# Kernel tuning notes

Measured on AMD Instinct MI355X. Metric: run time of the kernel, lower is better.

## Reference

```python
import jax, jax.numpy as jnp
import numpy as np

DIM = 256; SEQ = 2048; WIN = 64; HEADS = 4; RANK = 32; LAYERS = 3; VOCAB = 32000
EPS = 1e-6

def _unit(v):
    # unit_normalize_values: project onto unit sphere along feature dim
    return v / jnp.maximum(jnp.linalg.norm(v, axis=-1, keepdims=True), EPS)

def _signed_softmax(s):
    # signed_softmax_state: sign(s) * softmax(|s|) over nodes
    return jnp.sign(s) * jax.nn.softmax(jnp.abs(s), axis=-1)

def setup_inputs() -> dict:
    key = jax.random.key(0)
    ks = jax.random.split(key, 10)
    d = DIM
    return {
        "input_ids": jax.random.randint(ks[0], (2, SEQ), 0, VOCAB, dtype=jnp.int32),
        "emb": 0.02 * jax.random.normal(ks[1], (VOCAB, d), jnp.float32),
        "pos_emb": 0.02 * jax.random.normal(ks[2], (SEQ, d), jnp.float32),
        "anchor_val": 0.02 * jax.random.normal(ks[3], (d,), jnp.float32),
        "anchor_state": jnp.zeros((), jnp.float32),
        "Ws": 0.02 * jax.random.normal(ks[4], (d,), jnp.float32),
        "bs": jnp.zeros((), jnp.float32),
        "U": 0.02 * jax.random.normal(ks[5], (LAYERS, d, HEADS, RANK), jnp.float32),
        "V": 0.02 * jax.random.normal(ks[6], (LAYERS, d, HEADS, RANK), jnp.float32),
        "W1": 0.02 * jax.random.normal(ks[7], (LAYERS, d, 2 * d), jnp.float32),
        "b1": jnp.zeros((LAYERS, 2 * d), jnp.float32),
        "W2": 0.02 * jax.random.normal(ks[8], (LAYERS, 2 * d, d), jnp.float32),
        "b2": jnp.zeros((LAYERS, d), jnp.float32),
    }

def _forward(emb, pos_emb, anchor_val, anchor_state, Ws, bs, U, V, W1, b1, W2, b2, input_ids):
    B, S = input_ids.shape
    tok = emb[input_ids] + pos_emb[None, :S]          # [B,S,D]
    state_src = tok                                    # state projected from pre-unit-norm values
    tok = _unit(tok)
    tstate = state_src @ Ws + bs                       # [B,S] scalar state per node
    val = jnp.concatenate([jnp.broadcast_to(_unit(anchor_val), (B, 1, DIM)), tok], axis=1)
    state = jnp.concatenate([jnp.broadcast_to(anchor_state, (B, 1)), tstate], axis=1)
    N = S + 1
    offs = jnp.arange(-WIN, WIN + 1)
    idx = jnp.arange(N)[:, None] + offs[None, :]       # [N,K]
    valid = (idx >= 0) & (idx < N)
    idxc = jnp.clip(idx, 0, N - 1)
    inv_sqrt_r = np.float32(1.0 / np.sqrt(RANK))
    for l in range(LAYERS):
        q = jnp.einsum('bnd,dhr->bnhr', val, U[l])
        k = jnp.einsum('bnd,dhr->bnhr', val, V[l])
        knb = k[:, idxc]                               # [B,N,K,H,R] window gather
        s = jnp.einsum('bnhr,bnkhr->bnkh', q, knb) * inv_sqrt_r
        s = s.max(axis=-1)                             # max head-aggregate [B,N,K]
        a = jnp.where(valid, jnp.abs(s), -jnp.inf)
        wgt = jnp.where(valid, jnp.sign(s) * jax.nn.softmax(a, axis=-1), 0.0)  # signed-abs-softmax edges
        dval = jnp.einsum('bnk,bnkd->bnd', wgt, val[:, idxc])
        dstate = jnp.sum(wgt * state[:, idxc], axis=-1)
        # apply_delta: residual + norm(identity) + unit-norm + touched-mask where
        updated = val + dval
        nv = _unit(updated)
        touched = jnp.max(jnp.abs(jax.lax.stop_gradient(dval)), axis=-1, keepdims=True) > 0
        val = jnp.where(touched, nv, updated)
        state = _signed_softmax(state + dstate)
        # residual feed-forward then re-unit-norm
        h = jax.nn.gelu(jnp.einsum('bnd,dh->bnh', val, W1[l]) + b1[l], approximate=False)
        val = _unit(val + jnp.einsum('bnh,hd->bnd', h, W2[l]) + b2[l])
    return state, val

def reference(input_ids, emb, pos_emb, anchor_val, anchor_state, Ws, bs, U, V, W1, b1, W2, b2):
    return _forward(emb, pos_emb, anchor_val, anchor_state, Ws, bs, U, V, W1, b1, W2, b2, input_ids)
```

## Files before the change

### kernel.cpp

```cpp
#include <hip/hip_runtime.h>
#include <hip/hip_bf16.h>
#include <math.h>

#define BB 2
#define SS 2048
#define NN 2049
#define MM (BB*NN)
#define DD 256
#define HR 128
#define NHEAD 4
#define WINW 64
#define DFF 512
#define EPSF 1e-6f
#define TB8 257

typedef __attribute__((ext_vector_type(8))) short bf16x8;
typedef __attribute__((ext_vector_type(4))) float f32x4;

__device__ __forceinline__ float wave_sum(float v) {
    v += __shfl_down(v, 32, 64); v += __shfl_down(v, 16, 64);
    v += __shfl_down(v, 8, 64);  v += __shfl_down(v, 4, 64);
    v += __shfl_down(v, 2, 64);  v += __shfl_down(v, 1, 64);
    return v;
}
__device__ __forceinline__ float wave_max(float v) {
    v = fmaxf(v, __shfl_down(v, 32, 64)); v = fmaxf(v, __shfl_down(v, 16, 64));
    v = fmaxf(v, __shfl_down(v, 8, 64));  v = fmaxf(v, __shfl_down(v, 4, 64));
    v = fmaxf(v, __shfl_down(v, 2, 64));  v = fmaxf(v, __shfl_down(v, 1, 64));
    return v;
}
__device__ __forceinline__ float block_sum(float v, float* red) {
    v = wave_sum(v);
    __syncthreads();
    if ((threadIdx.x & 63) == 0) red[threadIdx.x >> 6] = v;
    __syncthreads();
    return red[0] + red[1] + red[2] + red[3];
}
__device__ __forceinline__ float sgnf(float x) {
    return (x > 0.f) ? 1.f : ((x < 0.f) ? -1.f : 0.f);
}
__device__ __forceinline__ ushort f2b(float x) {
    __hip_bfloat16 h = __float2bfloat16(x);
    return *(ushort*)&h;
}
__device__ __forceinline__ float b2f(ushort u) {
    unsigned int v = ((unsigned int)u) << 16;
    return *(float*)&v;
}
__device__ __forceinline__ void split3(float x, ushort& h, ushort& m, ushort& l) {
    h = f2b(x);
    float r1 = x - b2f(h);
    m = f2b(r1);
    l = f2b(r1 - b2f(m));
}
__device__ __forceinline__ void pack_map(int e, int N, int& k, int& n) {
    int j = e & 7;
    int l = (e >> 3) & 63;
    int c = e >> 9;
    int ntiles = N >> 4;
    int kt = c / ntiles, nt = c - kt * ntiles;
    k = kt * 32 + ((l >> 4) << 3) + j;
    n = nt * 16 + (l & 15);
}
__device__ __forceinline__ void dma16(const ushort* g, ushort* lds) {
    __builtin_amdgcn_global_load_lds(
        (const __attribute__((address_space(1))) unsigned int*)g,
        (__attribute__((address_space(3))) unsigned int*)lds,
        16, 0, 0);
}

__global__ void pre_kernel(const int* __restrict__ ids,
                           const float* __restrict__ emb,
                           const float* __restrict__ pos,
                           const float* __restrict__ anchor_val,
                           const float* __restrict__ anchor_state,
                           const float* __restrict__ Ws,
                           const float* __restrict__ bs,
                           float* __restrict__ val,
                           float* __restrict__ state,
                           const float* __restrict__ W1, const float* __restrict__ W2,
                           const float* __restrict__ U,  const float* __restrict__ V,
                           ushort* __restrict__ W1ph, ushort* __restrict__ W1pl,
                           ushort* __restrict__ W2ph, ushort* __restrict__ W2pl,
                           ushort* __restrict__ U0, ushort* __restrict__ U1,
                           ushort* __restrict__ U2,
                           ushort* __restrict__ V0, ushort* __restrict__ V1,
                           ushort* __restrict__ V2) {
    __shared__ float red[4];
    int bid = blockIdx.x;
    int t = threadIdx.x;
    if (bid < MM) {
        int b = bid / NN, n = bid % NN;
        float e;
        if (n == 0) {
            e = anchor_val[t];
        } else {
            int id = ids[b * SS + (n - 1)];
            e = emb[(size_t)id * DD + t] + pos[(size_t)(n - 1) * DD + t];
        }
        float ss = block_sum(e * e, red);
        float ts = block_sum(e * Ws[t], red);
        float rn = 1.f / fmaxf(sqrtf(ss), EPSF);
        float o = e * rn;
        val[(size_t)bid * DD + t] = o;
        if (t == 0) state[bid] = (n == 0) ? anchor_state[0] : (ts + bs[0]);
        return;
    }
    int idx = (bid - MM) * 256 + t;
    int l = idx / 327680;
    int r = idx - l * 327680;
    if (l >= 3) return;
    int k, n;
    if (r < 131072) {
        int e = r;
        pack_map(e, 512, k, n);
        float s = W1[(size_t)l * 131072 + (size_t)k * 512 + n];
        ushort h = f2b(s);
        W1ph[(size_t)l * 131072 + e] = h;
        W1pl[(size_t)l * 131072 + e] = f2b(s - b2f(h));
    } else if (r < 262144) {
        int e = r - 131072;
        pack_map(e, 256, k, n);
        float s = W2[(size_t)l * 131072 + (size_t)k * 256 + n];
        ushort h = f2b(s);
        W2ph[(size_t)l * 131072 + e] = h;
        W2pl[(size_t)l * 131072 + e] = f2b(s - b2f(h));
    } else if (r < 294912) {
        int e = r - 262144;
        pack_map(e, 128, k, n);
        ushort h, m, lo;
        split3(U[(size_t)l * 32768 + (size_t)k * 128 + n], h, m, lo);
        U0[(size_t)l * 32768 + e] = h;
        U1[(size_t)l * 32768 + e] = m;
        U2[(size_t)l * 32768 + e] = lo;
    } else {
        int e = r - 294912;
        pack_map(e, 128, k, n);
        ushort h, m, lo;
        split3(V[(size_t)l * 32768 + (size_t)k * 128 + n], h, m, lo);
        V0[(size_t)l * 32768 + e] = h;
        V1[(size_t)l * 32768 + e] = m;
        V2[(size_t)l * 32768 + e] = lo;
    }
}

__global__ __launch_bounds__(256, 2)
void proj_kernel(const float* __restrict__ Xin,
                 const ushort* __restrict__ U0, const ushort* __restrict__ U1,
                 const ushort* __restrict__ U2,
                 const ushort* __restrict__ V0, const ushort* __restrict__ V1,
                 const ushort* __restrict__ V2,
                 ushort* __restrict__ q0, ushort* __restrict__ q1,
                 ushort* __restrict__ q2,
                 ushort* __restrict__ k0, ushort* __restrict__ k1,
                 ushort* __restrict__ k2,
                 float* __restrict__ valG, int donorm) {
    __shared__ __align__(16) ushort stage[2][24 * 512];
    __shared__ __align__(16) ushort pln[3][16 * 256];
    int t = threadIdx.x;
    int w = t >> 6, l = t & 63;
    int lm = l & 15, quad = l >> 4;
    int m0 = blockIdx.x * 16;
    bool isQ = (blockIdx.y == 0);
    const ushort* P[3];
    P[0] = isQ ? U0 : V0;
    P[1] = isQ ? U1 : V1;
    P[2] = isQ ? U2 : V2;

    #pragma unroll
    for (int i = 0; i < 6; i++) {
        int c = w * 6 + i;
        int p = c >> 3, ntl = c & 7;
        dma16(P[p] + ((size_t)ntl * 64 + l) * 8,
              &stage[0][c * 512 + l * 8]);
    }
    asm volatile("" ::: "memory");

    #pragma unroll
    for (int rr = 0; rr < 4; rr++) {
        int row = w * 4 + rr;
        int tok = m0 + row; if (tok > MM - 1) tok = MM - 1;
        f32x4 x = *(const f32x4*)(Xin + (size_t)tok * DD + l * 4);
        if (donorm) {
            float s = x[0]*x[0] + x[1]*x[1] + x[2]*x[2] + x[3]*x[3];
            #pragma unroll
            for (int off = 1; off < 64; off <<= 1) s += __shfl_xor(s, off, 64);
            float rn = 1.f / fmaxf(sqrtf(s), EPSF);
            x[0] *= rn; x[1] *= rn; x[2] *= rn; x[3] *= rn;
            if (isQ) *(f32x4*)(valG + (size_t)tok * DD + l * 4) = x;
        }
        ushort4 h4, m4, l4;
        ushort hh, mm, ll;
        split3(x[0], hh, mm, ll); h4.x = hh; m4.x = mm; l4.x = ll;
        split3(x[1], hh, mm, ll); h4.y = hh; m4.y = mm; l4.y = ll;
        split3(x[2], hh, mm, ll); h4.z = hh; m4.z = mm; l4.z = ll;
        split3(x[3], hh, mm, ll); h4.w = hh; m4.w = mm; l4.w = ll;
        unsigned byte = ((unsigned)(row * 512 + l * 8)) ^ ((unsigned)((row & 7) << 4));
        *(ushort4*)((char*)&pln[0][0] + byte) = h4;
        *(ushort4*)((char*)&pln[1][0] + byte) = m4;
        *(ushort4*)((char*)&pln[2][0] + byte) = l4;
    }
    __syncthreads();

    f32x4 acc[2];
    acc[0] = (f32x4)(0.f); acc[1] = (f32x4)(0.f);
    #pragma unroll
    for (int kt = 0; kt < 8; kt++) {
        int cur = kt & 1;
        if (kt < 7) {
            #pragma unroll
            for (int i = 0; i < 6; i++) {
                int c = w * 6 + i;
                int p = c >> 3, ntl = c & 7;
                dma16(P[p] + ((size_t)((kt + 1) * 8 + ntl) * 64 + l) * 8,
                      &stage[cur ^ 1][c * 512 + l * 8]);
            }
            asm volatile("s_waitcnt vmcnt(6)" ::: "memory");
        } else {
            asm volatile("s_waitcnt vmcnt(0)" ::: "memory");
        }
        __builtin_amdgcn_s_barrier();
        unsigned abyte = ((unsigned)(lm * 512 + kt * 64 + quad * 16)) ^
                         ((unsigned)((lm & 7) << 4));
        bf16x8 a0 = *(const bf16x8*)((char*)&pln[0][0] + abyte);
        bf16x8 a1 = *(const bf16x8*)((char*)&pln[1][0] + abyte);
        bf16x8 a2 = *(const bf16x8*)((char*)&pln[2][0] + abyte);
        #pragma unroll
        for (int jj = 0; jj < 2; jj++) {
            int ntl = w * 2 + jj;
            bf16x8 b0 = *(const bf16x8*)&stage[cur][(0 * 8 + ntl) * 512 + l * 8];
            bf16x8 b1 = *(const bf16x8*)&stage[cur][(1 * 8 + ntl) * 512 + l * 8];
            bf16x8 b2 = *(const bf16x8*)&stage[cur][(2 * 8 + ntl) * 512 + l * 8];
            acc[jj] = __builtin_amdgcn_mfma_f32_16x16x32_bf16(a0, b0, acc[jj], 0, 0, 0);
            acc[jj] = __builtin_amdgcn_mfma_f32_16x16x32_bf16(a0, b1, acc[jj], 0, 0, 0);
            acc[jj] = __builtin_amdgcn_mfma_f32_16x16x32_bf16(a1, b0, acc[jj], 0, 0, 0);
            acc[jj] = __builtin_amdgcn_mfma_f32_16x16x32_bf16(a1, b1, acc[jj], 0, 0, 0);
            acc[jj] = __builtin_amdgcn_mfma_f32_16x16x32_bf16(a0, b2, acc[jj], 0, 0, 0);
            acc[jj] = __builtin_amdgcn_mfma_f32_16x16x32_bf16(a2, b0, acc[jj], 0, 0, 0);
        }
        __builtin_amdgcn_s_barrier();
    }
    ushort* o0 = isQ ? q0 : k0;
    ushort* o1 = isQ ? q1 : k1;
    ushort* o2 = isQ ? q2 : k2;
    #pragma unroll
    for (int jj = 0; jj < 2; jj++) {
        int n = (w * 2 + jj) * 16 + lm;
        #pragma unroll
        for (int r = 0; r < 4; r++) {
            int tok = m0 + quad * 4 + r;
            if (tok < MM) {
                ushort h, m, lo;
                split3(acc[jj][r], h, m, lo);
                size_t oi = (size_t)tok * HR + n;
                o0[oi] = h; o1[oi] = m; o2[oi] = lo;
            }
        }
    }
}

__global__ __launch_bounds__(256, 2)
void attn_kernel(const float* __restrict__ val_in,
                 const float* __restrict__ state_in,
                 const ushort* __restrict__ q0, const ushort* __restrict__ q1,
                 const ushort* __restrict__ q2,
                 const ushort* __restrict__ k0, const ushort* __restrict__ k1,
                 const ushort* __restrict__ k2,
                 float* __restrict__ val_out,
                 ushort* __restrict__ vbH, ushort* __restrict__ vbM,
                 float* __restrict__ dstate_out) {
    __shared__ float sc4[NHEAD][8][148];
    __shared__ float wgt2[144][12];
    __shared__ float redS[8][4];
    __shared__ float redM[8][4];

    int b = blockIdx.x / TB8;
    int n0 = (blockIdx.x % TB8) * 8;
    int t = threadIdx.x;
    int w = t >> 6, l = t & 63;
    int lm = l & 15, quad = l >> 4;

    {
        int qrow = n0 + (lm & 7);
        if (qrow > NN - 1) qrow = NN - 1;
        size_t qa = ((size_t)(b * NN + qrow)) * HR + w * 32 + quad * 8;
        bf16x8 a0 = *(const bf16x8*)(q0 + qa);
        bf16x8 a1 = *(const bf16x8*)(q1 + qa);
        bf16x8 a2 = *(const bf16x8*)(q2 + qa);
        bf16x8 kf0[9], kf1[9], kf2[9];
        #pragma unroll
        for (int jt = 0; jt < 9; jt++) {
            int j = n0 - 64 + jt * 16 + lm;
            j = (j < 0) ? 0 : ((j > NN - 1) ? NN - 1 : j);
            size_t ka = ((size_t)(b * NN + j)) * HR + w * 32 + quad * 8;
            kf0[jt] = *(const bf16x8*)(k0 + ka);
            kf1[jt] = *(const bf16x8*)(k1 + ka);
            kf2[jt] = *(const bf16x8*)(k2 + ka);
        }
        #pragma unroll
        for (int jt = 0; jt < 9; jt++) {
            f32x4 acc = (f32x4)(0.f);
            acc = __builtin_amdgcn_mfma_f32_16x16x32_bf16(a0, kf0[jt], acc, 0, 0, 0);
            acc = __builtin_amdgcn_mfma_f32_16x16x32_bf16(a0, kf1[jt], acc, 0, 0, 0);
            acc = __builtin_amdgcn_mfma_f32_16x16x32_bf16(a1, kf0[jt], acc, 0, 0, 0);
            acc = __builtin_amdgcn_mfma_f32_16x16x32_bf16(a1, kf1[jt], acc, 0, 0, 0);
            acc = __builtin_amdgcn_mfma_f32_16x16x32_bf16(a0, kf2[jt], acc, 0, 0, 0);
            acc = __builtin_amdgcn_mfma_f32_16x16x32_bf16(a2, kf0[jt], acc, 0, 0, 0);
            if (quad < 2) {
                #pragma unroll
                for (int r = 0; r < 4; r++)
                    sc4[w][quad * 4 + r][jt * 16 + lm] = acc[r];
            }
        }
    }
    __syncthreads();

    {
        int m = t >> 5, p = t & 31;
        int n = n0 + m;
        bool tokv = (n < NN);
        float sv[5]; bool vv[5];
        float mx = -INFINITY;
        #pragma unroll
        for (int i = 0; i < 5; i++) {
            int tap = p + 32 * i;
            bool inb = (tap < 144);
            int tapc = inb ? tap : 0;
            int j = n0 - 64 + tapc;
            float s0 = sc4[0][m][tapc], s1 = sc4[1][m][tapc];
            float s2 = sc4[2][m][tapc], s3 = sc4[3][m][tapc];
            float s = fmaxf(fmaxf(s0, s1), fmaxf(s2, s3)) * 0.17677669529663687f;
            bool v = inb && tokv && (tap >= m) && (tap <= m + 128) && (j >= 0) && (j < NN);
            sv[i] = s; vv[i] = v;
            if (v) mx = fmaxf(mx, fabsf(s));
        }
        for (int off = 16; off > 0; off >>= 1) mx = fmaxf(mx, __shfl_xor(mx, off, 64));
        float ee[5];
        float sum = 0.f;
        #pragma unroll
        for (int i = 0; i < 5; i++) {
            ee[i] = vv[i] ? expf(fabsf(sv[i]) - mx) : 0.f;
            sum += ee[i];
        }
        for (int off = 16; off > 0; off >>= 1) sum += __shfl_xor(sum, off, 64);
        float inv = (sum > 0.f) ? 1.f / sum : 0.f;
        float ds = 0.f;
        #pragma unroll
        for (int i = 0; i < 5; i++) {
            int tap = p + 32 * i;
            if (tap < 144) {
                float wg = vv[i] ? sgnf(sv[i]) * ee[i] * inv : 0.f;
                wgt2[tap][m] = wg;
                if (vv[i]) ds += wg * state_in[b * NN + (n0 - 64 + tap)];
            }
        }
        for (int off = 16; off > 0; off >>= 1) ds += __shfl_xor(ds, off, 64);
        if (p == 0 && tokv) dstate_out[b * NN + n] = ds;
    }
    __syncthreads();

    {
        int d = (t >> 2) * 4;
        int tg = t & 3;
        int tok0 = tg * 2, tok1 = tg * 2 + 1;
        int jlo = (n0 >= 64) ? 0 : (64 - n0);
        int jhi = NN - 1 - n0 + 64; if (jhi > 135) jhi = 135;
        const float* vbase = val_in + ((size_t)(b * NN + n0 - 64)) * DD + d;
        f32x4 acc0 = (f32x4)(0.f), acc1 = (f32x4)(0.f);
        int jj = jlo;
        for (; jj + 3 <= jhi; jj += 4) {
            f32x4 v0 = *(const f32x4*)(vbase + (size_t)(jj + 0) * DD);
            f32x4 v1 = *(const f32x4*)(vbase + (size_t)(jj + 1) * DD);
            f32x4 v2 = *(const f32x4*)(vbase + (size_t)(jj + 2) * DD);
            f32x4 v3 = *(const f32x4*)(vbase + (size_t)(jj + 3) * DD);
            float wa0 = wgt2[jj + 0][tok0], wa1 = wgt2[jj + 0][tok1];
            float wb0 = wgt2[jj + 1][tok0], wb1 = wgt2[jj + 1][tok1];
            float wc0 = wgt2[jj + 2][tok0], wc1 = wgt2[jj + 2][tok1];
            float wd0 = wgt2[jj + 3][tok0], wd1 = wgt2[jj + 3][tok1];
            #pragma unroll
            for (int c = 0; c < 4; c++) {
                acc0[c] += v0[c] * wa0 + v1[c] * wb0 + v2[c] * wc0 + v3[c] * wd0;
                acc1[c] += v0[c] * wa1 + v1[c] * wb1 + v2[c] * wc1 + v3[c] * wd1;
            }
        }
        for (; jj <= jhi; jj++) {
            f32x4 v = *(const f32x4*)(vbase + (size_t)jj * DD);
            float w0 = wgt2[jj][tok0], w1 = wgt2[jj][tok1];
            #pragma unroll
            for (int c = 0; c < 4; c++) {
                acc0[c] += v[c] * w0;
                acc1[c] += v[c] * w1;
            }
        }
        f32x4 u[2]; f32x4 ac[2]; ac[0] = acc0; ac[1] = acc1;
        #pragma unroll
        for (int ti = 0; ti < 2; ti++) {
            int tok = tg * 2 + ti;
            int n = n0 + tok;
            f32x4 vold = (f32x4)(0.f);
            if (n < NN) vold = *(const f32x4*)(val_in + ((size_t)(b * NN + n)) * DD + d);
            u[ti] = vold + ac[ti];
            float s = u[ti][0]*u[ti][0] + u[ti][1]*u[ti][1] + u[ti][2]*u[ti][2] + u[ti][3]*u[ti][3];
            float mb = fmaxf(fmaxf(fabsf(ac[ti][0]), fabsf(ac[ti][1])),
                             fmaxf(fabsf(ac[ti][2]), fabsf(ac[ti][3])));
            for (int off = 4; off <= 32; off <<= 1) {
                s += __shfl_xor(s, off, 64);
                mb = fmaxf(mb, __shfl_xor(mb, off, 64));
            }
            if ((l >> 2) == 0) { redS[tok][w] = s; redM[tok][w] = mb; }
        }
        __syncthreads();
        #pragma unroll
        for (int ti = 0; ti < 2; ti++) {
            int tok = tg * 2 + ti;
            int n = n0 + tok;
            if (n < NN) {
                float ss = redS[tok][0] + redS[tok][1] + redS[tok][2] + redS[tok][3];
                float mab = fmaxf(fmaxf(redM[tok][0], redM[tok][1]),
                                  fmaxf(redM[tok][2], redM[tok][3]));
                float rn = 1.f / fmaxf(sqrtf(ss), EPSF);
                f32x4 o = u[ti];
                if (mab > 0.f) { o[0] *= rn; o[1] *= rn; o[2] *= rn; o[3] *= rn; }
                size_t oi = ((size_t)(b * NN + n)) * DD + d;
                *(f32x4*)(val_out + oi) = o;
                ushort4 hv, mv;
                {
                    ushort h0 = f2b(o[0]); hv.x = h0; mv.x = f2b(o[0] - b2f(h0));
                    ushort h1 = f2b(o[1]); hv.y = h1; mv.y = f2b(o[1] - b2f(h1));
                    ushort h2 = f2b(o[2]); hv.z = h2; mv.z = f2b(o[2] - b2f(h2));
                    ushort h3 = f2b(o[3]); hv.w = h3; mv.w = f2b(o[3] - b2f(h3));
                }
                *(ushort4*)(vbH + oi) = hv;
                *(ushort4*)(vbM + oi) = mv;
            }
        }
    }
}

__global__ __launch_bounds__(256, 2)
void ffn1_kernel(const ushort* __restrict__ XbH, const ushort* __restrict__ XbM,
                 const ushort* __restrict__ W1h, const ushort* __restrict__ W1l,
                 const float*  __restrict__ b1,
                 ushort* __restrict__ Hh, ushort* __restrict__ Hl,
                 const float* __restrict__ state_in, const float* __restrict__ dstate,
                 float* __restrict__ state_out) {
    __shared__ __align__(16) ushort stage[2][32 * 512];
    int t = threadIdx.x;

    if (blockIdx.x == 257) {
        float* red = (float*)&stage[0][0];
        int b = blockIdx.y;
        float lmax = -INFINITY;
        for (int n = t; n < NN; n += 256) {
            float x = state_in[b * NN + n] + dstate[b * NN + n];
            lmax = fmaxf(lmax, fabsf(x));
        }
        lmax = wave_max(lmax);
        if ((t & 63) == 0) red[t >> 6] = lmax;
        __syncthreads();
        float m = fmaxf(fmaxf(red[0], red[1]), fmaxf(red[2], red[3]));
        float lsum = 0.f;
        for (int n = t; n < NN; n += 256)
            lsum += expf(fabsf(state_in[b * NN + n] + dstate[b * NN + n]) - m);
        lsum = wave_sum(lsum);
        __syncthreads();
        if ((t & 63) == 0) red[4 + (t >> 6)] = lsum;
        __syncthreads();
        float inv = 1.f / (red[4] + red[5] + red[6] + red[7]);
        for (int n = t; n < NN; n += 256) {
            float x = state_in[b * NN + n] + dstate[b * NN + n];
            state_out[b * NN + n] = sgnf(x) * expf(fabsf(x) - m) * inv;
        }
        return;
    }

    int w = t >> 6, l = t & 63;
    int lm = l & 15, quad = l >> 4;
    int m0 = blockIdx.x * 16;
    int nh = blockIdx.y;
    int row0 = m0 + lm; if (row0 > MM - 1) row0 = MM - 1;
    const ushort* xh = XbH + (size_t)row0 * DD + quad * 8;
    const ushort* xm = XbM + (size_t)row0 * DD + quad * 8;

    bf16x8 ah[2], am[2];
    ah[0] = *(const bf16x8*)(xh);
    am[0] = *(const bf16x8*)(xm);
    #pragma unroll
    for (int i = 0; i < 8; i++) {
        int c = w * 8 + i;
        int p = c >> 4, ntl = c & 15;
        const ushort* src = (p ? W1l : W1h) + ((size_t)(nh * 16 + ntl) * 64 + l) * 8;
        dma16(src, &stage[0][c * 512 + l * 8]);
    }
    asm volatile("" ::: "memory");

    f32x4 acc[4];
    #pragma unroll
    for (int jj = 0; jj < 4; jj++) acc[jj] = (f32x4)(0.f);

    #pragma unroll
    for (int kt = 0; kt < 8; kt++) {
        int cur = kt & 1;
        if (kt < 7) {
            ah[cur ^ 1] = *(const bf16x8*)(xh + (kt + 1) * 32);
            am[cur ^ 1] = *(const bf16x8*)(xm + (kt + 1) * 32);
            #pragma unroll
            for (int i = 0; i < 8; i++) {
                int c = w * 8 + i;
                int p = c >> 4, ntl = c & 15;
                const ushort* src = (p ? W1l : W1h) +
                    ((size_t)((kt + 1) * 32 + nh * 16 + ntl) * 64 + l) * 8;
                dma16(src, &stage[cur ^ 1][c * 512 + l * 8]);
            }
            asm volatile("s_waitcnt vmcnt(10)" ::: "memory");
        } else {
            asm volatile("s_waitcnt vmcnt(0)" ::: "memory");
        }
        __builtin_amdgcn_s_barrier();
        #pragma unroll
        for (int jj = 0; jj < 4; jj++) {
            int ntl = w * 4 + jj;
            bf16x8 bh = *(const bf16x8*)&stage[cur][ntl * 512 + l * 8];
            bf16x8 bl = *(const bf16x8*)&stage[cur][(16 + ntl) * 512 + l * 8];
            acc[jj] = __builtin_amdgcn_mfma_f32_16x16x32_bf16(ah[cur], bh, acc[jj], 0, 0, 0);
            acc[jj] = __builtin_amdgcn_mfma_f32_16x16x32_bf16(am[cur], bh, acc[jj], 0, 0, 0);
            acc[jj] = __builtin_amdgcn_mfma_f32_16x16x32_bf16(ah[cur], bl, acc[jj], 0, 0, 0);
        }
        __builtin_amdgcn_s_barrier();
    }
    #pragma unroll
    for (int jj = 0; jj < 4; jj++) {
        int gn = nh * 256 + (w * 4 + jj) * 16 + lm;
        float bb = b1[gn];
        #pragma unroll
        for (int r = 0; r < 4; r++) {
            int tok = m0 + quad * 4 + r;
            if (tok < MM) {
                float x = acc[jj][r] + bb;
                float g = 0.5f * x * (1.f + erff(x * 0.70710678118654752f));
                ushort gh = f2b(g);
                size_t oi = (size_t)tok * DFF + gn;
                Hh[oi] = gh;
                Hl[oi] = f2b(g - b2f(gh));
            }
        }
    }
}

__global__ __launch_bounds__(256, 2)
void ffn2_kernel(const ushort* __restrict__ Hh, const ushort* __restrict__ Hl,
                 const float*  __restrict__ Xf,
                 const ushort* __restrict__ W2h, const ushort* __restrict__ W2l,
                 const float*  __restrict__ b2,
                 float* __restrict__ Yb) {
    __shared__ __align__(16) ushort stage[2][16 * 512];
    int t = threadIdx.x;
    int w = t >> 6, l = t & 63;
    int lm = l & 15, quad = l >> 4;
    int m0 = blockIdx.x * 16;
    int nh = blockIdx.y;
    int row0 = m0 + lm; if (row0 > MM - 1) row0 = MM - 1;
    const ushort* xh = Hh + (size_t)row0 * DFF + quad * 8;
    const ushort* xl = Hl + (size_t)row0 * DFF + quad * 8;

    bf16x8 ah[2], al[2];
    ah[0] = *(const bf16x8*)(xh);
    al[0] = *(const bf16x8*)(xl);
    #pragma unroll
    for (int i = 0; i < 4; i++) {
        int c = w * 4 + i;
        int p = c >> 3, ntl = c & 7;
        const ushort* src = (p ? W2l : W2h) + ((size_t)(nh * 8 + ntl) * 64 + l) * 8;
        dma16(src, &stage[0][c * 512 + l * 8]);
    }
    asm volatile("" ::: "memory");

    f32x4 acc[2];
    acc[0] = (f32x4)(0.f); acc[1] = (f32x4)(0.f);

    #pragma unroll
    for (int kt = 0; kt < 16; kt++) {
        int cur = kt & 1;
        if (kt < 15) {
            ah[cur ^ 1] = *(const bf16x8*)(xh + (kt + 1) * 32);
            al[cur ^ 1] = *(const bf16x8*)(xl + (kt + 1) * 32);
            #pragma unroll
            for (int i = 0; i < 4; i++) {
                int c = w * 4 + i;
                int p = c >> 3, ntl = c & 7;
                const ushort* src = (p ? W2l : W2h) +
                    ((size_t)((kt + 1) * 16 + nh * 8 + ntl) * 64 + l) * 8;
                dma16(src, &stage[cur ^ 1][c * 512 + l * 8]);
            }
            asm volatile("s_waitcnt vmcnt(6)" ::: "memory");
        } else {
            asm volatile("s_waitcnt vmcnt(0)" ::: "memory");
        }
        __builtin_amdgcn_s_barrier();
        #pragma unroll
        for (int jj = 0; jj < 2; jj++) {
            int ntl = w * 2 + jj;
            bf16x8 bh = *(const bf16x8*)&stage[cur][ntl * 512 + l * 8];
            bf16x8 bl = *(const bf16x8*)&stage[cur][(8 + ntl) * 512 + l * 8];
            acc[jj] = __builtin_amdgcn_mfma_f32_16x16x32_bf16(ah[cur], bh, acc[jj], 0, 0, 0);
            acc[jj] = __builtin_amdgcn_mfma_f32_16x16x32_bf16(al[cur], bh, acc[jj], 0, 0, 0);
            acc[jj] = __builtin_amdgcn_mfma_f32_16x16x32_bf16(ah[cur], bl, acc[jj], 0, 0, 0);
        }
        __builtin_amdgcn_s_barrier();
    }
    #pragma unroll
    for (int jj = 0; jj < 2; jj++) {
        int gn = nh * 128 + (w * 2 + jj) * 16 + lm;
        float bb = b2[gn];
        #pragma unroll
        for (int r = 0; r < 4; r++) {
            int tok = m0 + quad * 4 + r;
            if (tok < MM) {
                size_t oi = (size_t)tok * DD + gn;
                Yb[oi] = Xf[oi] + acc[jj][r] + bb;
            }
        }
    }
}

__global__ void ffn3f_kernel(const float* __restrict__ Yb,
                             float* __restrict__ val_out) {
    int t = threadIdx.x;
    int w = t >> 6, l = t & 63;
    int row = blockIdx.x * 4 + w;
    if (row >= MM) return;
    f32x4 y = *(const f32x4*)(Yb + (size_t)row * DD + l * 4);
    float s = y[0]*y[0] + y[1]*y[1] + y[2]*y[2] + y[3]*y[3];
    #pragma unroll
    for (int off = 1; off < 64; off <<= 1) s += __shfl_xor(s, off, 64);
    float rn = 1.f / fmaxf(sqrtf(s), EPSF);
    f32x4 o;
    o[0] = y[0] * rn; o[1] = y[1] * rn; o[2] = y[2] * rn; o[3] = y[3] * rn;
    *(f32x4*)(val_out + (size_t)row * DD + l * 4) = o;
}

extern "C" void kernel_launch(void* const* d_in, const int* in_sizes, int n_in,
                              void* d_out, int out_size, void* d_ws, size_t ws_size,
                              hipStream_t stream) {
    const int*   ids          = (const int*)d_in[0];
    const float* emb          = (const float*)d_in[1];
    const float* pos          = (const float*)d_in[2];
    const float* anchor_val   = (const float*)d_in[3];
    const float* anchor_state = (const float*)d_in[4];
    const float* Ws           = (const float*)d_in[5];
    const float* bs           = (const float*)d_in[6];
    const float* U            = (const float*)d_in[7];
    const float* V            = (const float*)d_in[8];
    const float* W1           = (const float*)d_in[9];
    const float* b1           = (const float*)d_in[10];
    const float* W2           = (const float*)d_in[11];
    const float* b2           = (const float*)d_in[12];
    float* out = (float*)d_out;

    ushort* p = (ushort*)d_ws;
    ushort* vB0 = p; p += (size_t)MM * DD;
    ushort* vB1 = p; p += (size_t)MM * DD;
    ushort* q0b = p; p += (size_t)MM * HR;
    ushort* q1b = p; p += (size_t)MM * HR;
    ushort* q2b = p; p += (size_t)MM * HR;
    ushort* k0b = p; p += (size_t)MM * HR;
    ushort* k1b = p; p += (size_t)MM * HR;
    ushort* k2b = p; p += (size_t)MM * HR;
    ushort* Hh  = p; p += (size_t)MM * DFF;
    ushort* Hl  = p; p += (size_t)MM * DFF;
    ushort* W1ph = p; p += 3 * 131072;
    ushort* W1pl = p; p += 3 * 131072;
    ushort* W2ph = p; p += 3 * 131072;
    ushort* W2pl = p; p += 3 * 131072;
    ushort* U0p = p; p += 3 * 32768;
    ushort* U1p = p; p += 3 * 32768;
    ushort* U2p = p; p += 3 * 32768;
    ushort* V0p = p; p += 3 * 32768;
    ushort* V1p = p; p += 3 * 32768;
    ushort* V2p = p; p += 3 * 32768;
    float* f = (float*)p;
    float* valA = f; f += (size_t)MM * DD;
    float* valB = f; f += (size_t)MM * DD;
    float* Yb   = f; f += (size_t)MM * DD;
    float* st0  = f; f += MM;
    float* st1  = f; f += MM;
    float* dst  = f; f += MM;

    pre_kernel<<<MM + 3840, 256, 0, stream>>>(ids, emb, pos, anchor_val, anchor_state,
                                              Ws, bs, valA, st0,
                                              W1, W2, U, V,
                                              W1ph, W1pl, W2ph, W2pl,
                                              U0p, U1p, U2p, V0p, V1p, V2p);
    float* s_in = st0;
    float* s_out = st1;
    for (int l = 0; l < 3; l++) {
        const float* Xin = (l == 0) ? valA : Yb;
        proj_kernel<<<dim3(257, 2), 256, 0, stream>>>(
            Xin,
            U0p + (size_t)l * 32768, U1p + (size_t)l * 32768, U2p + (size_t)l * 32768,
            V0p + (size_t)l * 32768, V1p + (size_t)l * 32768, V2p + (size_t)l * 32768,
            q0b, q1b, q2b, k0b, k1b, k2b,
            valA, (l == 0) ? 0 : 1);
        attn_kernel<<<BB * TB8, 256, 0, stream>>>(valA, s_in,
                                                  q0b, q1b, q2b, k0b, k1b, k2b,
                                                  valB, vB0, vB1, dst);
        ffn1_kernel<<<dim3(258, 2), 256, 0, stream>>>(
            vB0, vB1,
            W1ph + (size_t)l * 131072, W1pl + (size_t)l * 131072, b1 + (size_t)l * DFF,
            Hh, Hl,
            s_in, dst, (l == 2) ? out : s_out);
        ffn2_kernel<<<dim3(257, 2), 256, 0, stream>>>(
            Hh, Hl, valB,
            W2ph + (size_t)l * 131072, W2pl + (size_t)l * 131072, b2 + (size_t)l * DD,
            Yb);
        float* tmp = s_in; s_in = s_out; s_out = tmp;
    }
    ffn3f_kernel<<<(MM + 3) / 4, 256, 0, stream>>>(Yb, out + MM);
}
```

Measured before the change: 351.3 us.

## Drop LDS staging of weights; load MFMA B-fragments directly from global

Removes the double-buffered global_load_lds staging of pre-packed weight tiles in the proj, ffn1 and ffn2 kernels. Each wave now reads its B fragments straight from global memory, relying on L2/cache reuse since every wave reads distinct fragments anyway. This drops the per-iteration barriers and shared-memory footprint, and launch bounds are raised to allow more resident blocks. The attention kernel also stops preloading all nine K tiles into registers and loads them per tile. The cost is that global-load latency is no longer explicitly prefetched, so the kernels depend on occupancy to hide it.

```diff
diff --git a/kernel.cpp b/kernel.cpp
--- a/kernel.cpp
+++ b/kernel.cpp
@@ -61,12 +61,6 @@
     int kt = c / ntiles, nt = c - kt * ntiles;
     k = kt * 32 + ((l >> 4) << 3) + j;
     n = nt * 16 + (l & 15);
-}
-__device__ __forceinline__ void dma16(const ushort* g, ushort* lds) {
-    __builtin_amdgcn_global_load_lds(
-        (const __attribute__((address_space(1))) unsigned int*)g,
-        (__attribute__((address_space(3))) unsigned int*)lds,
-        16, 0, 0);
 }
 
 __global__ void pre_kernel(const int* __restrict__ ids,
@@ -144,7 +138,7 @@
     }
 }
 
-__global__ __launch_bounds__(256, 2)
+__global__ __launch_bounds__(256, 3)
 void proj_kernel(const float* __restrict__ Xin,
                  const ushort* __restrict__ U0, const ushort* __restrict__ U1,
                  const ushort* __restrict__ U2,
@@ -155,26 +149,15 @@
                  ushort* __restrict__ k0, ushort* __restrict__ k1,
                  ushort* __restrict__ k2,
                  float* __restrict__ valG, int donorm) {
-    __shared__ __align__(16) ushort stage[2][24 * 512];
     __shared__ __align__(16) ushort pln[3][16 * 256];
     int t = threadIdx.x;
     int w = t >> 6, l = t & 63;
     int lm = l & 15, quad = l >> 4;
     int m0 = blockIdx.x * 16;
     bool isQ = (blockIdx.y == 0);
-    const ushort* P[3];
-    P[0] = isQ ? U0 : V0;
-    P[1] = isQ ? U1 : V1;
-    P[2] = isQ ? U2 : V2;
-
-    #pragma unroll
-    for (int i = 0; i < 6; i++) {
-        int c = w * 6 + i;
-        int p = c >> 3, ntl = c & 7;
-        dma16(P[p] + ((size_t)ntl * 64 + l) * 8,
-              &stage[0][c * 512 + l * 8]);
-    }
-    asm volatile("" ::: "memory");
+    const ushort* P0 = isQ ? U0 : V0;
+    const ushort* P1 = isQ ? U1 : V1;
+    const ushort* P2 = isQ ? U2 : V2;
 
     #pragma unroll
     for (int rr = 0; rr < 4; rr++) {
@@ -206,20 +189,6 @@
     acc[0] = (f32x4)(0.f); acc[1] = (f32x4)(0.f);
     #pragma unroll
     for (int kt = 0; kt < 8; kt++) {
-        int cur = kt & 1;
-        if (kt < 7) {
-            #pragma unroll
-            for (int i = 0; i < 6; i++) {
-                int c = w * 6 + i;
-                int p = c >> 3, ntl = c & 7;
-                dma16(P[p] + ((size_t)((kt + 1) * 8 + ntl) * 64 + l) * 8,
-                      &stage[cur ^ 1][c * 512 + l * 8]);
-            }
-            asm volatile("s_waitcnt vmcnt(6)" ::: "memory");
-        } else {
-            asm volatile("s_waitcnt vmcnt(0)" ::: "memory");
-        }
-        __builtin_amdgcn_s_barrier();
         unsigned abyte = ((unsigned)(lm * 512 + kt * 64 + quad * 16)) ^
                          ((unsigned)((lm & 7) << 4));
         bf16x8 a0 = *(const bf16x8*)((char*)&pln[0][0] + abyte);
@@ -228,9 +197,10 @@
         #pragma unroll
         for (int jj = 0; jj < 2; jj++) {
             int ntl = w * 2 + jj;
-            bf16x8 b0 = *(const bf16x8*)&stage[cur][(0 * 8 + ntl) * 512 + l * 8];
-            bf16x8 b1 = *(const bf16x8*)&stage[cur][(1 * 8 + ntl) * 512 + l * 8];
-            bf16x8 b2 = *(const bf16x8*)&stage[cur][(2 * 8 + ntl) * 512 + l * 8];
+            size_t off = ((size_t)(kt * 8 + ntl) * 64 + l) * 8;
+            bf16x8 b0 = *(const bf16x8*)(P0 + off);
+            bf16x8 b1 = *(const bf16x8*)(P1 + off);
+            bf16x8 b2 = *(const bf16x8*)(P2 + off);
             acc[jj] = __builtin_amdgcn_mfma_f32_16x16x32_bf16(a0, b0, acc[jj], 0, 0, 0);
             acc[jj] = __builtin_amdgcn_mfma_f32_16x16x32_bf16(a0, b1, acc[jj], 0, 0, 0);
             acc[jj] = __builtin_amdgcn_mfma_f32_16x16x32_bf16(a1, b0, acc[jj], 0, 0, 0);
@@ -238,7 +208,6 @@
             acc[jj] = __builtin_amdgcn_mfma_f32_16x16x32_bf16(a0, b2, acc[jj], 0, 0, 0);
             acc[jj] = __builtin_amdgcn_mfma_f32_16x16x32_bf16(a2, b0, acc[jj], 0, 0, 0);
         }
-        __builtin_amdgcn_s_barrier();
     }
     ushort* o0 = isQ ? q0 : k0;
     ushort* o1 = isQ ? q1 : k1;
@@ -259,7 +228,7 @@
     }
 }
 
-__global__ __launch_bounds__(256, 2)
+__global__ __launch_bounds__(256, 3)
 void attn_kernel(const float* __restrict__ val_in,
                  const float* __restrict__ state_in,
                  const ushort* __restrict__ q0, const ushort* __restrict__ q1,
@@ -287,25 +256,21 @@
         bf16x8 a0 = *(const bf16x8*)(q0 + qa);
         bf16x8 a1 = *(const bf16x8*)(q1 + qa);
         bf16x8 a2 = *(const bf16x8*)(q2 + qa);
-        bf16x8 kf0[9], kf1[9], kf2[9];
         #pragma unroll
         for (int jt = 0; jt < 9; jt++) {
             int j = n0 - 64 + jt * 16 + lm;
             j = (j < 0) ? 0 : ((j > NN - 1) ? NN - 1 : j);
             size_t ka = ((size_t)(b * NN + j)) * HR + w * 32 + quad * 8;
-            kf0[jt] = *(const bf16x8*)(k0 + ka);
-            kf1[jt] = *(const bf16x8*)(k1 + ka);
-            kf2[jt] = *(const bf16x8*)(k2 + ka);
-        }
-        #pragma unroll
-        for (int jt = 0; jt < 9; jt++) {
+            bf16x8 kf0 = *(const bf16x8*)(k0 + ka);
+            bf16x8 kf1 = *(const bf16x8*)(k1 + ka);
+            bf16x8 kf2 = *(const bf16x8*)(k2 + ka);
             f32x4 acc = (f32x4)(0.f);
-            acc = __builtin_amdgcn_mfma_f32_16x16x32_bf16(a0, kf0[jt], acc, 0, 0, 0);
-            acc = __builtin_amdgcn_mfma_f32_16x16x32_bf16(a0, kf1[jt], acc, 0, 0, 0);
-            acc = __builtin_amdgcn_mfma_f32_16x16x32_bf16(a1, kf0[jt], acc, 0, 0, 0);
-            acc = __builtin_amdgcn_mfma_f32_16x16x32_bf16(a1, kf1[jt], acc, 0, 0, 0);
-            acc = __builtin_amdgcn_mfma_f32_16x16x32_bf16(a0, kf2[jt], acc, 0, 0, 0);
-            acc = __builtin_amdgcn_mfma_f32_16x16x32_bf16(a2, kf0[jt], acc, 0, 0, 0);
+            acc = __builtin_amdgcn_mfma_f32_16x16x32_bf16(a0, kf0, acc, 0, 0, 0);
+            acc = __builtin_amdgcn_mfma_f32_16x16x32_bf16(a0, kf1, acc, 0, 0, 0);
+            acc = __builtin_amdgcn_mfma_f32_16x16x32_bf16(a1, kf0, acc, 0, 0, 0);
+            acc = __builtin_amdgcn_mfma_f32_16x16x32_bf16(a1, kf1, acc, 0, 0, 0);
+            acc = __builtin_amdgcn_mfma_f32_16x16x32_bf16(a0, kf2, acc, 0, 0, 0);
+            acc = __builtin_amdgcn_mfma_f32_16x16x32_bf16(a2, kf0, acc, 0, 0, 0);
             if (quad < 2) {
                 #pragma unroll
                 for (int r = 0; r < 4; r++)
@@ -437,18 +402,17 @@
     }
 }
 
-__global__ __launch_bounds__(256, 2)
+__global__ __launch_bounds__(256, 3)
 void ffn1_kernel(const ushort* __restrict__ XbH, const ushort* __restrict__ XbM,
                  const ushort* __restrict__ W1h, const ushort* __restrict__ W1l,
                  const float*  __restrict__ b1,
                  ushort* __restrict__ Hh, ushort* __restrict__ Hl,
                  const float* __restrict__ state_in, const float* __restrict__ dstate,
                  float* __restrict__ state_out) {
-    __shared__ __align__(16) ushort stage[2][32 * 512];
+    __shared__ float red[8];
     int t = threadIdx.x;
 
     if (blockIdx.x == 257) {
-        float* red = (float*)&stage[0][0];
         int b = blockIdx.y;
         float lmax = -INFINITY;
         for (int n = t; n < NN; n += 256) {
@@ -482,51 +446,24 @@
     const ushort* xh = XbH + (size_t)row0 * DD + quad * 8;
     const ushort* xm = XbM + (size_t)row0 * DD + quad * 8;
 
-    bf16x8 ah[2], am[2];
-    ah[0] = *(const bf16x8*)(xh);
-    am[0] = *(const bf16x8*)(xm);
-    #pragma unroll
-    for (int i = 0; i < 8; i++) {
-        int c = w * 8 + i;
-        int p = c >> 4, ntl = c & 15;
-        const ushort* src = (p ? W1l : W1h) + ((size_t)(nh * 16 + ntl) * 64 + l) * 8;
-        dma16(src, &stage[0][c * 512 + l * 8]);
-    }
-    asm volatile("" ::: "memory");
-
     f32x4 acc[4];
     #pragma unroll
     for (int jj = 0; jj < 4; jj++) acc[jj] = (f32x4)(0.f);
 
     #pragma unroll
     for (int kt = 0; kt < 8; kt++) {
-        int cur = kt & 1;
-        if (kt < 7) {
-            ah[cur ^ 1] = *(const bf16x8*)(xh + (kt + 1) * 32);
-            am[cur ^ 1] = *(const bf16x8*)(xm + (kt + 1) * 32);
-            #pragma unroll
-            for (int i = 0; i < 8; i++) {
-                int c = w * 8 + i;
-                int p = c >> 4, ntl = c & 15;
-                const ushort* src = (p ? W1l : W1h) +
-                    ((size_t)((kt + 1) * 32 + nh * 16 + ntl) * 64 + l) * 8;
-                dma16(src, &stage[cur ^ 1][c * 512 + l * 8]);
-            }
-            asm volatile("s_waitcnt vmcnt(10)" ::: "memory");
-        } else {
-            asm volatile("s_waitcnt vmcnt(0)" ::: "memory");
-        }
-        __builtin_amdgcn_s_barrier();
+        bf16x8 ah = *(const bf16x8*)(xh + kt * 32);
+        bf16x8 am = *(const bf16x8*)(xm + kt * 32);
         #pragma unroll
         for (int jj = 0; jj < 4; jj++) {
             int ntl = w * 4 + jj;
-            bf16x8 bh = *(const bf16x8*)&stage[cur][ntl * 512 + l * 8];
-            bf16x8 bl = *(const bf16x8*)&stage[cur][(16 + ntl) * 512 + l * 8];
-            acc[jj] = __builtin_amdgcn_mfma_f32_16x16x32_bf16(ah[cur], bh, acc[jj], 0, 0, 0);
-            acc[jj] = __builtin_amdgcn_mfma_f32_16x16x32_bf16(am[cur], bh, acc[jj], 0, 0, 0);
-            acc[jj] = __builtin_amdgcn_mfma_f32_16x16x32_bf16(ah[cur], bl, acc[jj], 0, 0, 0);
-        }
-        __builtin_amdgcn_s_barrier();
+            size_t off = ((size_t)(kt * 32 + nh * 16 + ntl) * 64 + l) * 8;
+            bf16x8 bh = *(const bf16x8*)(W1h + off);
+            bf16x8 bl = *(const bf16x8*)(W1l + off);
+            acc[jj] = __builtin_amdgcn_mfma_f32_16x16x32_bf16(ah, bh, acc[jj], 0, 0, 0);
+            acc[jj] = __builtin_amdgcn_mfma_f32_16x16x32_bf16(am, bh, acc[jj], 0, 0, 0);
+            acc[jj] = __builtin_amdgcn_mfma_f32_16x16x32_bf16(ah, bl, acc[jj], 0, 0, 0);
+        }
     }
     #pragma unroll
     for (int jj = 0; jj < 4; jj++) {
@@ -547,13 +484,12 @@
     }
 }
 
-__global__ __launch_bounds__(256, 2)
+__global__ __launch_bounds__(256, 4)
 void ffn2_kernel(const ushort* __restrict__ Hh, const ushort* __restrict__ Hl,
                  const float*  __restrict__ Xf,
                  const ushort* __restrict__ W2h, const ushort* __restrict__ W2l,
                  const float*  __restrict__ b2,
                  float* __restrict__ Yb) {
-    __shared__ __align__(16) ushort stage[2][16 * 512];
     int t = threadIdx.x;
     int w = t >> 6, l = t & 63;
     int lm = l & 15, quad = l >> 4;
@@ -563,50 +499,23 @@
     const ushort* xh = Hh + (size_t)row0 * DFF + quad * 8;
     const ushort* xl = Hl + (size_t)row0 * DFF + quad * 8;
 
-    bf16x8 ah[2], al[2];
-    ah[0] = *(const bf16x8*)(xh);
-    al[0] = *(const bf16x8*)(xl);
-    #pragma unroll
-    for (int i = 0; i < 4; i++) {
-        int c = w * 4 + i;
-        int p = c >> 3, ntl = c & 7;
-        const ushort* src = (p ? W2l : W2h) + ((size_t)(nh * 8 + ntl) * 64 + l) * 8;
-        dma16(src, &stage[0][c * 512 + l * 8]);
-    }
-    asm volatile("" ::: "memory");
-
     f32x4 acc[2];
     acc[0] = (f32x4)(0.f); acc[1] = (f32x4)(0.f);
 
     #pragma unroll
     for (int kt = 0; kt < 16; kt++) {
-        int cur = kt & 1;
-        if (kt < 15) {
-            ah[cur ^ 1] = *(const bf16x8*)(xh + (kt + 1) * 32);
-            al[cur ^ 1] = *(const bf16x8*)(xl + (kt + 1) * 32);
-            #pragma unroll
-            for (int i = 0; i < 4; i++) {
-                int c = w * 4 + i;
-                int p = c >> 3, ntl = c & 7;
-                const ushort* src = (p ? W2l : W2h) +
-                    ((size_t)((kt + 1) * 16 + nh * 8 + ntl) * 64 + l) * 8;
-                dma16(src, &stage[cur ^ 1][c * 512 + l * 8]);
-            }
-            asm volatile("s_waitcnt vmcnt(6)" ::: "memory");
-        } else {
-            asm volatile("s_waitcnt vmcnt(0)" ::: "memory");
-        }
-        __builtin_amdgcn_s_barrier();
+        bf16x8 ah = *(const bf16x8*)(xh + kt * 32);
+        bf16x8 al = *(const bf16x8*)(xl + kt * 32);
         #pragma unroll
         for (int jj = 0; jj < 2; jj++) {
             int ntl = w * 2 + jj;
-            bf16x8 bh = *(const bf16x8*)&stage[cur][ntl * 512 + l * 8];
-            bf16x8 bl = *(const bf16x8*)&stage[cur][(8 + ntl) * 512 + l * 8];
-            acc[jj] = __builtin_amdgcn_mfma_f32_16x16x32_bf16(ah[cur], bh, acc[jj], 0, 0, 0);
-            acc[jj] = __builtin_amdgcn_mfma_f32_16x16x32_bf16(al[cur], bh, acc[jj], 0, 0, 0);
-            acc[jj] = __builtin_amdgcn_mfma_f32_16x16x32_bf16(ah[cur], bl, acc[jj], 0, 0, 0);
-        }
-        __builtin_amdgcn_s_barrier();
+            size_t off = ((size_t)(kt * 16 + nh * 8 + ntl) * 64 + l) * 8;
+            bf16x8 bh = *(const bf16x8*)(W2h + off);
+            bf16x8 bl = *(const bf16x8*)(W2l + off);
+            acc[jj] = __builtin_amdgcn_mfma_f32_16x16x32_bf16(ah, bh, acc[jj], 0, 0, 0);
+            acc[jj] = __builtin_amdgcn_mfma_f32_16x16x32_bf16(al, bh, acc[jj], 0, 0, 0);
+            acc[jj] = __builtin_amdgcn_mfma_f32_16x16x32_bf16(ah, bl, acc[jj], 0, 0, 0);
+        }
     }
     #pragma unroll
     for (int jj = 0; jj < 2; jj++) {
```

Measured after the change: 360.0 us. +2.5%, slower.
